# Kernel tuning notes

Measured on AMD Instinct MI355X. Metric: run time of the kernel, lower is better.

The kernel has to match this reference:

```python
import jax, jax.numpy as jnp
import numpy as np

D_MODEL = 1024
N_HEADS = 16
D_K = D_MODEL // N_HEADS


def setup_inputs() -> dict:
    key = jax.random.key(0)
    ks = jax.random.split(key, 10)
    B, S = 4, 2048
    scale = 1.0 / np.sqrt(D_MODEL)
    inp = {
        "x": jax.random.normal(ks[0], (B, S, D_MODEL), dtype=jnp.float32),
        "mask": jnp.ones((B, S), dtype=jnp.int32),
        "w_q": jax.random.normal(ks[1], (D_MODEL, D_MODEL), dtype=jnp.float32) * scale,
        "b_q": jnp.zeros((D_MODEL,), dtype=jnp.float32),
        "w_k": jax.random.normal(ks[2], (D_MODEL, D_MODEL), dtype=jnp.float32) * scale,
        "b_k": jnp.zeros((D_MODEL,), dtype=jnp.float32),
        "w_v": jax.random.normal(ks[3], (D_MODEL, D_MODEL), dtype=jnp.float32) * scale,
        "b_v": jnp.zeros((D_MODEL,), dtype=jnp.float32),
        "w_o": jax.random.normal(ks[4], (D_MODEL, D_MODEL), dtype=jnp.float32) * scale,
        "b_o": jnp.zeros((D_MODEL,), dtype=jnp.float32),
    }
    return inp


def reference(x, mask, w_q, b_q, w_k, b_k, w_v, b_v, w_o, b_o):
    B, S, _ = x.shape
    # projections; weights stored (in, out) so x @ W + b
    def proj(w, b):
        return (x @ w + b).reshape(B, S, N_HEADS, D_K).transpose(0, 2, 1, 3)  # [B,H,S,Dk]
    Q = proj(w_q, b_q)
    K = proj(w_k, b_k)
    V = proj(w_v, b_v)
    scores = jnp.einsum("bhqd,bhkd->bhqk", Q, K) / np.sqrt(D_K)  # [B,H,S,S]
    # mask: (B,S) -> (B,1,1,S); masked positions set to -1e9 (matches masked_fill)
    scores = jnp.where(mask[:, None, None, :] == 0, jnp.float32(-1e9), scores)
    attn = jax.nn.softmax(scores, axis=-1)
    # dropout is identity at inference (eval mode)
    context = jnp.einsum("bhqk,bhkd->bhqd", attn, V)  # [B,H,S,Dk]
    context = context.transpose(0, 2, 1, 3).reshape(B, S, D_MODEL)
    return context @ w_o + b_o
```

## Files before the change

kernel.cpp:

```cpp
#include <hip/hip_runtime.h>

typedef __attribute__((ext_vector_type(8)))  short short8;
typedef __attribute__((ext_vector_type(4)))  float f32x4;
typedef __attribute__((ext_vector_type(16))) float f32x16;

__device__ __forceinline__ short f2b(float f) {
    union { float f; unsigned u; } v; v.f = f;
    unsigned r = v.u + 0x7FFF + ((v.u >> 16) & 1);
    return (short)(r >> 16);
}

__device__ __forceinline__ float fexp2(float x) {
    float r;
    asm("v_exp_f32 %0, %1" : "=v"(r) : "v"(x));
    return r;
}

__device__ __forceinline__ void gll16(const void* g, void* l) {
    __builtin_amdgcn_global_load_lds(
        (const __attribute__((address_space(1))) void*)g,
        (__attribute__((address_space(3))) void*)l, 16, 0, 0);
}


__global__ __launch_bounds__(256) void xconv_kernel(const float4* __restrict__ X,
                                                    short* __restrict__ xb) {
    int i = blockIdx.x * 256 + threadIdx.x;
    float4 v = X[i];
    short4 o;
    o.x = f2b(v.x); o.y = f2b(v.y); o.z = f2b(v.z); o.w = f2b(v.w);
    ((short4*)xb)[i] = o;
}

__global__ __launch_bounds__(256) void wconv4_kernel(
    const float* __restrict__ w0, const float* __restrict__ w1,
    const float* __restrict__ w2, const float* __restrict__ w3,
    short* __restrict__ wqkvt, short* __restrict__ wot) {
    __shared__ float t[32][33];
    int z = blockIdx.z;
    const float* W = (z == 0) ? w0 : (z == 1) ? w1 : (z == 2) ? w2 : w3;
    short* WT = (z < 3) ? wqkvt : wot;
    int row_off = (z < 3) ? z * 1024 : 0;
    int bx = blockIdx.x, by = blockIdx.y;
    int c = threadIdx.x & 31, r0 = threadIdx.x >> 5;
    #pragma unroll
    for (int p = 0; p < 4; ++p) {
        int r = r0 + p * 8;
        t[r][c] = W[(size_t)(by * 32 + r) * 1024 + bx * 32 + c];
    }
    __syncthreads();
    #pragma unroll
    for (int p = 0; p < 4; ++p) {
        int r = r0 + p * 8;
        WT[(size_t)(row_off + bx * 32 + r) * 1024 + by * 32 + c] = f2b(t[c][r]);
    }
}

__global__ __launch_bounds__(256) void vtrans_kernel(const short* __restrict__ V,
                                                     short* __restrict__ Vt) {
    __shared__ short t[64][72];
    int st = blockIdx.x, bh = blockIdx.y;
    const size_t vbase = (size_t)bh * 2048 * 64;
    const size_t tbase = (size_t)bh * 64 * 2048;
    int tid = threadIdx.x;
    #pragma unroll
    for (int p = 0; p < 16; ++p) {
        int e = p * 256 + tid;
        int r = e >> 6, c = e & 63;
        t[r][c] = V[vbase + (size_t)(st * 64 + r) * 64 + c];
    }
    __syncthreads();
    #pragma unroll
    for (int p = 0; p < 16; ++p) {
        int e = p * 256 + tid;
        int d = e >> 6, c = e & 63;
        Vt[tbase + (size_t)d * 2048 + st * 64 + c] = t[c][d];
    }
}

__global__ __launch_bounds__(256) void mfma_gemm_kernel(
    const short* __restrict__ A, const short* __restrict__ Bt,
    const float* __restrict__ b0, const float* __restrict__ b1,
    const float* __restrict__ b2,
    short* __restrict__ Qo, short* __restrict__ Ko, short* __restrict__ Vo,
    float* __restrict__ Co, int K, int mode)
{
    __shared__ __align__(16) short As[2][128 * 32];
    __shared__ __align__(16) short Bs[2][128 * 32];

    const int tid = threadIdx.x;
    const int lane = tid & 63;
    const int w = tid >> 6;
    const int quad = lane >> 4;
    const int l15 = lane & 15;
    const int wm = (w & 1) * 64;
    const int wn = (w >> 1) * 64;
    const int m0 = blockIdx.y * 128;
    const int n0 = blockIdx.x * 128;

    const int rl = lane >> 2;
    const int cl = lane & 3;
    const short* srcA[2]; const short* srcB[2];
    int doff[2];
    #pragma unroll
    for (int t = 0; t < 2; ++t) {
        int row = w * 32 + t * 16 + rl;
        int sc = cl ^ (row & 3);
        srcA[t] = A  + (size_t)(m0 + row) * K + sc * 8;
        srcB[t] = Bt + (size_t)(n0 + row) * K + sc * 8;
        doff[t] = (w * 32 + t * 16) * 32;
    }

    int offA[4], offB[4];
    #pragma unroll
    for (int i = 0; i < 4; ++i) {
        int m = wm + i * 16 + l15;
        offA[i] = m * 32 + ((quad ^ (m & 3)) * 8);
        int n = wn + i * 16 + l15;
        offB[i] = n * 32 + ((quad ^ (n & 3)) * 8);
    }

    f32x4 acc[4][4];
    #pragma unroll
    for (int i = 0; i < 4; ++i)
        #pragma unroll
        for (int j = 0; j < 4; ++j)
            acc[i][j] = (f32x4){0.f, 0.f, 0.f, 0.f};

    #pragma unroll
    for (int t = 0; t < 2; ++t) {
        gll16(srcA[t], As[0] + doff[t]);
        gll16(srcB[t], Bs[0] + doff[t]);
    }
    __syncthreads();

    const int KT = K >> 5;
    for (int kt = 0; kt < KT; ++kt) {
        if (kt + 1 < KT) {
            int k1 = (kt + 1) << 5;
            int nb = (kt + 1) & 1;
            #pragma unroll
            for (int t = 0; t < 2; ++t) {
                gll16(srcA[t] + k1, As[nb] + doff[t]);
                gll16(srcB[t] + k1, Bs[nb] + doff[t]);
            }
        }
        const short* as = As[kt & 1];
        const short* bs = Bs[kt & 1];
        short8 af[4], bfr[4];
        #pragma unroll
        for (int i = 0; i < 4; ++i) af[i] = *(const short8*)(as + offA[i]);
        #pragma unroll
        for (int j = 0; j < 4; ++j) bfr[j] = *(const short8*)(bs + offB[j]);
        #pragma unroll
        for (int i = 0; i < 4; ++i)
            #pragma unroll
            for (int j = 0; j < 4; ++j)
                acc[i][j] = __builtin_amdgcn_mfma_f32_16x16x32_bf16(af[i], bfr[j], acc[i][j], 0, 0, 0);
        __syncthreads();
    }

    #pragma unroll
    for (int j = 0; j < 4; ++j) {
        int ng = n0 + wn + j * 16 + l15;
        if (mode == 0) {
            int mat = ng >> 10;
            int nl = ng & 1023;
            float bv = (mat == 0) ? b0[nl] : (mat == 1) ? b1[nl] : b2[nl];
            short* dst = (mat == 0) ? Qo : (mat == 1) ? Ko : Vo;
            float scl = (mat == 0) ? 0.18033688011112042f : 1.0f;
            int hh = nl >> 6, dd = nl & 63;
            #pragma unroll
            for (int i = 0; i < 4; ++i)
                #pragma unroll
                for (int r = 0; r < 4; ++r) {
                    int mg = m0 + wm + i * 16 + quad * 4 + r;
                    int bb = mg >> 11, ss = mg & 2047;
                    dst[(((size_t)(bb * 16 + hh)) * 2048 + ss) * 64 + dd] = f2b((acc[i][j][r] + bv) * scl);
                }
        } else {
            float bv = b0[ng];
            #pragma unroll
            for (int i = 0; i < 4; ++i)
                #pragma unroll
                for (int r = 0; r < 4; ++r) {
                    int mg = m0 + wm + i * 16 + quad * 4 + r;
                    Co[(size_t)mg * 1024 + ng] = acc[i][j][r] + bv;
                }
        }
    }
}

__global__ __launch_bounds__(256) void attn_mfma_kernel(
    const short* __restrict__ Q, const short* __restrict__ Kg,
    const short* __restrict__ Vt, const int* __restrict__ mask,
    short* __restrict__ ctx)
{
    __shared__ __align__(16) short Ks[2][64 * 64];
    __shared__ __align__(16) short Vs[2][64 * 64];
    __shared__ int msks[2][64];
    __shared__ float Linv[4][32];

    const int tid = threadIdx.x;
    const int lane = tid & 63;
    const int w = tid >> 6;
    const int l31 = lane & 31;
    const int hi = lane >> 5;
    const int bh = blockIdx.x;
    const int q0 = blockIdx.y * 128;
    const int h = bh & 15;
    const int b = bh >> 4;
    const size_t qkbase = (size_t)bh * 2048 * 64;
    const size_t vtbase = (size_t)bh * 64 * 2048;

    const int rl8 = lane >> 3;
    const int cl8 = lane & 7;

    const short* srcK[2]; const short* srcV[2];
    int dstoff[2];
    #pragma unroll
    for (int t = 0; t < 2; ++t) {
        int row = w * 16 + t * 8 + rl8;
        int sc = cl8 ^ (row & 7);
        srcK[t] = Kg + qkbase + (size_t)row * 64 + sc * 8;
        srcV[t] = Vt + vtbase + (size_t)row * 2048 + sc * 8;
        dstoff[t] = (w * 16 + t * 8) * 64;
    }

    #pragma unroll
    for (int t = 0; t < 2; ++t) {
        gll16(srcK[t], Ks[0] + dstoff[t]);
        gll16(srcV[t], Vs[0] + dstoff[t]);
    }
    if (tid < 64) msks[0][tid] = mask[b * 2048 + tid];

    short8 qf[4];
    {
        const short* qptr = Q + qkbase + (size_t)(q0 + w * 32 + l31) * 64;
        #pragma unroll
        for (int s = 0; s < 4; ++s)
            qf[s] = *(const short8*)(qptr + (((s << 1) | hi)) * 8);
    }

    f32x16 o[2];
    #pragma unroll
    for (int ch = 0; ch < 2; ++ch)
        #pragma unroll
        for (int r = 0; r < 16; ++r) o[ch][r] = 0.f;
    float lsum = 0.f;

    __syncthreads();

    for (int t = 0; t < 32; ++t) {
        const int bidx = t & 1;
        if (t + 1 < 32) {
            const int nb = (t + 1) & 1;
            const int kt1 = (t + 1) * 64;
            #pragma unroll
            for (int s = 0; s < 2; ++s) {
                gll16(srcK[s] + (size_t)kt1 * 64, Ks[nb] + dstoff[s]);
                gll16(srcV[s] + kt1, Vs[nb] + dstoff[s]);
            }
            if (tid < 64) msks[nb][tid] = mask[b * 2048 + kt1 + tid];
        }

        const short* ks = Ks[bidx];
        const short* vs = Vs[bidx];
        unsigned long long bz = __ballot(msks[bidx][tid & 63] == 0);

        #pragma unroll
        for (int km = 0; km < 2; ++km) {
            f32x16 sa;
            #pragma unroll
            for (int r = 0; r < 16; ++r) sa[r] = 0.f;
            const int kr = km * 32 + l31;
            #pragma unroll
            for (int s = 0; s < 4; ++s) {
                short8 ka = *(const short8*)(ks + kr * 64 + (((s << 1) | hi) ^ (l31 & 7)) * 8);
                sa = __builtin_amdgcn_mfma_f32_32x32x16_bf16(ka, qf[s], sa, 0, 0, 0);
            }
            float ps[16];
            #pragma unroll
            for (int r = 0; r < 16; ++r) ps[r] = fexp2(sa[r]);
            if (bz) {
                #pragma unroll
                for (int r = 0; r < 16; ++r) {
                    int key = km * 32 + (r & 3) + 8 * (r >> 2) + 4 * hi;
                    if (msks[bidx][key] == 0) ps[r] = 0.f;
                }
            }
            #pragma unroll
            for (int r = 0; r < 16; ++r) lsum += ps[r];

            unsigned pk[8];
            #pragma unroll
            for (int c = 0; c < 8; ++c) {
                unsigned u0 = __builtin_bit_cast(unsigned, ps[2 * c])     + 0x8000u;
                unsigned u1 = __builtin_bit_cast(unsigned, ps[2 * c + 1]) + 0x8000u;
                pk[c] = __builtin_amdgcn_perm(u1, u0, 0x07060302u);
            }
            unsigned sk[8];
            #pragma unroll
            for (int c = 0; c < 8; ++c) sk[c] = (unsigned)__shfl_xor((int)pk[c], 32);

            uint4 A1u, A2u;
            A1u.x = hi ? sk[2] : pk[0];
            A1u.y = hi ? sk[3] : pk[1];
            A1u.z = hi ? pk[2] : sk[0];
            A1u.w = hi ? pk[3] : sk[1];
            A2u.x = hi ? sk[6] : pk[4];
            A2u.y = hi ? sk[7] : pk[5];
            A2u.z = hi ? pk[6] : sk[4];
            A2u.w = hi ? pk[7] : sk[5];
            short8 A1 = __builtin_bit_cast(short8, A1u);
            short8 A2 = __builtin_bit_cast(short8, A2u);

            #pragma unroll
            for (int ch = 0; ch < 2; ++ch) {
                const int d = ch * 32 + l31;
                short8 vb0 = *(const short8*)(vs + d * 64 + (((km * 4) | hi) ^ (d & 7)) * 8);
                short8 vb1 = *(const short8*)(vs + d * 64 + (((km * 4 + 2) | hi) ^ (d & 7)) * 8);
                o[ch] = __builtin_amdgcn_mfma_f32_32x32x16_bf16(A1, vb0, o[ch], 0, 0, 0);
                o[ch] = __builtin_amdgcn_mfma_f32_32x32x16_bf16(A2, vb1, o[ch], 0, 0, 0);
            }
        }
        __syncthreads();
    }

    float ltot = lsum + __shfl_xor(lsum, 32);
    if (hi == 0) Linv[w][l31] = 1.0f / ltot;
    asm volatile("s_waitcnt lgkmcnt(0)" ::: "memory");
    float invr[16];
    #pragma unroll
    for (int r = 0; r < 16; ++r)
        invr[r] = Linv[w][(r & 3) + 8 * (r >> 2) + 4 * hi];
    #pragma unroll
    for (int ch = 0; ch < 2; ++ch)
        #pragma unroll
        for (int r = 0; r < 16; ++r) {
            int rowq = (r & 3) + 8 * (r >> 2) + 4 * hi;
            int qg = q0 + w * 32 + rowq;
            ctx[((size_t)b * 2048 + qg) * 1024 + h * 64 + ch * 32 + l31] =
                f2b(o[ch][r] * invr[r]);
        }
}


extern "C" void kernel_launch(void* const* d_in, const int* in_sizes, int n_in,
                              void* d_out, int out_size, void* d_ws, size_t ws_size,
                              hipStream_t stream) {
    const size_t ME = (size_t)8192 * 1024;

    char* ws = (char*)d_ws;
    short* xb    = (short*)ws; ws += ME * 2;
    short* wqkvt = (short*)ws; ws += (size_t)3072 * 1024 * 2;
    short* wot   = (short*)ws; ws += (size_t)1024 * 1024 * 2;
    short* Qb    = (short*)ws; ws += ME * 2;
    short* Kb    = (short*)ws; ws += ME * 2;
    short* Vb    = (short*)ws; ws += ME * 2;
    short* Vt    = (short*)ws; ws += ME * 2;

    xconv_kernel<<<8192, 256, 0, stream>>>((const float4*)d_in[0], xb);
    wconv4_kernel<<<dim3(32, 32, 4), 256, 0, stream>>>(
        (const float*)d_in[2], (const float*)d_in[4],
        (const float*)d_in[6], (const float*)d_in[8], wqkvt, wot);

    mfma_gemm_kernel<<<dim3(24, 64), 256, 0, stream>>>(
        xb, wqkvt, (const float*)d_in[3], (const float*)d_in[5], (const float*)d_in[7],
        Qb, Kb, Vb, nullptr, 1024, 0);

    vtrans_kernel<<<dim3(32, 64), 256, 0, stream>>>(Vb, Vt);

    attn_mfma_kernel<<<dim3(64, 16), 256, 0, stream>>>(
        Qb, Kb, Vt, (const int*)d_in[1], xb );

    mfma_gemm_kernel<<<dim3(8, 64), 256, 0, stream>>>(
        xb, wot, (const float*)d_in[9], nullptr, nullptr,
        nullptr, nullptr, nullptr, (float*)d_out, 1024, 1);
}
```

Measured before the change: 339.9 us.

## Load attention K/V fragments directly from global and bit-pack the mask

Drops the double-buffered LDS staging of K and V tiles in the attention kernel. Each wave now reads its MFMA operands straight from global memory, relying on cache reuse across the four waves, and the block-wide barriers go away. The mask is packed into 32-bit words by a new small kernel, so each key tile needs one scalar word instead of an LDS mask array. The final row normalisation uses lane shuffles instead of LDS. The risk is more global/L2 traffic and exposed load latency, since there is no explicit prefetch.

```diff
diff --git a/kernel.cpp b/kernel.cpp
--- a/kernel.cpp
+++ b/kernel.cpp
@@ -8,12 +8,6 @@
     union { float f; unsigned u; } v; v.f = f;
     unsigned r = v.u + 0x7FFF + ((v.u >> 16) & 1);
     return (short)(r >> 16);
-}
-
-__device__ __forceinline__ float fexp2(float x) {
-    float r;
-    asm("v_exp_f32 %0, %1" : "=v"(r) : "v"(x));
-    return r;
 }
 
 __device__ __forceinline__ void gll16(const void* g, void* l) {
@@ -78,6 +72,16 @@
     }
 }
 
+__global__ __launch_bounds__(256) void maskpack_kernel(const int* __restrict__ mask,
+                                                       unsigned* __restrict__ mbits) {
+    int idx = blockIdx.x * 256 + threadIdx.x;
+    int lane = threadIdx.x & 63;
+    int m = mask[idx];
+    unsigned long long bal = __ballot(m != 0);
+    if ((lane & 31) == 0)
+        mbits[idx >> 5] = (unsigned)(bal >> ((lane >> 5) * 32));
+}
+
 __global__ __launch_bounds__(256) void mfma_gemm_kernel(
     const short* __restrict__ A, const short* __restrict__ Bt,
     const float* __restrict__ b0, const float* __restrict__ b1,
@@ -193,14 +197,9 @@
 
 __global__ __launch_bounds__(256) void attn_mfma_kernel(
     const short* __restrict__ Q, const short* __restrict__ Kg,
-    const short* __restrict__ Vt, const int* __restrict__ mask,
+    const short* __restrict__ Vt, const unsigned* __restrict__ mbits,
     short* __restrict__ ctx)
 {
-    __shared__ __align__(16) short Ks[2][64 * 64];
-    __shared__ __align__(16) short Vs[2][64 * 64];
-    __shared__ int msks[2][64];
-    __shared__ float Linv[4][32];
-
     const int tid = threadIdx.x;
     const int lane = tid & 63;
     const int w = tid >> 6;
@@ -213,34 +212,17 @@
     const size_t qkbase = (size_t)bh * 2048 * 64;
     const size_t vtbase = (size_t)bh * 64 * 2048;
 
-    const int rl8 = lane >> 3;
-    const int cl8 = lane & 7;
-
-    const short* srcK[2]; const short* srcV[2];
-    int dstoff[2];
-    #pragma unroll
-    for (int t = 0; t < 2; ++t) {
-        int row = w * 16 + t * 8 + rl8;
-        int sc = cl8 ^ (row & 7);
-        srcK[t] = Kg + qkbase + (size_t)row * 64 + sc * 8;
-        srcV[t] = Vt + vtbase + (size_t)row * 2048 + sc * 8;
-        dstoff[t] = (w * 16 + t * 8) * 64;
-    }
-
-    #pragma unroll
-    for (int t = 0; t < 2; ++t) {
-        gll16(srcK[t], Ks[0] + dstoff[t]);
-        gll16(srcV[t], Vs[0] + dstoff[t]);
-    }
-    if (tid < 64) msks[0][tid] = mask[b * 2048 + tid];
-
     short8 qf[4];
     {
-        const short* qptr = Q + qkbase + (size_t)(q0 + w * 32 + l31) * 64;
+        const short* qptr = Q + qkbase + (size_t)(q0 + w * 32 + l31) * 64 + hi * 8;
         #pragma unroll
         for (int s = 0; s < 4; ++s)
-            qf[s] = *(const short8*)(qptr + (((s << 1) | hi)) * 8);
-    }
+            qf[s] = *(const short8*)(qptr + s * 16);
+    }
+
+    const short* kbase  = Kg + qkbase + (size_t)l31 * 64 + hi * 8;
+    const short* vbase0 = Vt + vtbase + (size_t)(l31) * 2048 + hi * 8;
+    const short* vbase1 = Vt + vtbase + (size_t)(32 + l31) * 2048 + hi * 8;
 
     f32x16 o[2];
     #pragma unroll
@@ -249,99 +231,80 @@
         for (int r = 0; r < 16; ++r) o[ch][r] = 0.f;
     float lsum = 0.f;
 
-    __syncthreads();
-
-    for (int t = 0; t < 32; ++t) {
-        const int bidx = t & 1;
-        if (t + 1 < 32) {
-            const int nb = (t + 1) & 1;
-            const int kt1 = (t + 1) * 64;
-            #pragma unroll
-            for (int s = 0; s < 2; ++s) {
-                gll16(srcK[s] + (size_t)kt1 * 64, Ks[nb] + dstoff[s]);
-                gll16(srcV[s] + kt1, Vs[nb] + dstoff[s]);
+    for (int kt = 0; kt < 2048; kt += 32) {
+        unsigned mword = mbits[(b << 6) + (kt >> 5)];
+
+        const short* kp = kbase + (size_t)kt * 64;
+        f32x16 sa;
+        #pragma unroll
+        for (int r = 0; r < 16; ++r) sa[r] = 0.f;
+        #pragma unroll
+        for (int s = 0; s < 4; ++s) {
+            short8 ka = *(const short8*)(kp + s * 16);
+            sa = __builtin_amdgcn_mfma_f32_32x32x16_bf16(ka, qf[s], sa, 0, 0, 0);
+        }
+
+        float ps[16];
+        #pragma unroll
+        for (int r = 0; r < 16; ++r) ps[r] = __builtin_amdgcn_exp2f(sa[r]);
+        if (mword != 0xffffffffu) {
+            #pragma unroll
+            for (int r = 0; r < 16; ++r) {
+                int key = (r & 3) + 8 * (r >> 2) + 4 * hi;
+                if (!((mword >> key) & 1)) ps[r] = 0.f;
             }
-            if (tid < 64) msks[nb][tid] = mask[b * 2048 + kt1 + tid];
-        }
-
-        const short* ks = Ks[bidx];
-        const short* vs = Vs[bidx];
-        unsigned long long bz = __ballot(msks[bidx][tid & 63] == 0);
-
-        #pragma unroll
-        for (int km = 0; km < 2; ++km) {
-            f32x16 sa;
-            #pragma unroll
-            for (int r = 0; r < 16; ++r) sa[r] = 0.f;
-            const int kr = km * 32 + l31;
-            #pragma unroll
-            for (int s = 0; s < 4; ++s) {
-                short8 ka = *(const short8*)(ks + kr * 64 + (((s << 1) | hi) ^ (l31 & 7)) * 8);
-                sa = __builtin_amdgcn_mfma_f32_32x32x16_bf16(ka, qf[s], sa, 0, 0, 0);
-            }
-            float ps[16];
-            #pragma unroll
-            for (int r = 0; r < 16; ++r) ps[r] = fexp2(sa[r]);
-            if (bz) {
-                #pragma unroll
-                for (int r = 0; r < 16; ++r) {
-                    int key = km * 32 + (r & 3) + 8 * (r >> 2) + 4 * hi;
-                    if (msks[bidx][key] == 0) ps[r] = 0.f;
-                }
-            }
-            #pragma unroll
-            for (int r = 0; r < 16; ++r) lsum += ps[r];
-
-            unsigned pk[8];
-            #pragma unroll
-            for (int c = 0; c < 8; ++c) {
-                unsigned u0 = __builtin_bit_cast(unsigned, ps[2 * c])     + 0x8000u;
-                unsigned u1 = __builtin_bit_cast(unsigned, ps[2 * c + 1]) + 0x8000u;
-                pk[c] = __builtin_amdgcn_perm(u1, u0, 0x07060302u);
-            }
-            unsigned sk[8];
-            #pragma unroll
-            for (int c = 0; c < 8; ++c) sk[c] = (unsigned)__shfl_xor((int)pk[c], 32);
-
-            uint4 A1u, A2u;
-            A1u.x = hi ? sk[2] : pk[0];
-            A1u.y = hi ? sk[3] : pk[1];
-            A1u.z = hi ? pk[2] : sk[0];
-            A1u.w = hi ? pk[3] : sk[1];
-            A2u.x = hi ? sk[6] : pk[4];
-            A2u.y = hi ? sk[7] : pk[5];
-            A2u.z = hi ? pk[6] : sk[4];
-            A2u.w = hi ? pk[7] : sk[5];
-            short8 A1 = __builtin_bit_cast(short8, A1u);
-            short8 A2 = __builtin_bit_cast(short8, A2u);
-
-            #pragma unroll
-            for (int ch = 0; ch < 2; ++ch) {
-                const int d = ch * 32 + l31;
-                short8 vb0 = *(const short8*)(vs + d * 64 + (((km * 4) | hi) ^ (d & 7)) * 8);
-                short8 vb1 = *(const short8*)(vs + d * 64 + (((km * 4 + 2) | hi) ^ (d & 7)) * 8);
-                o[ch] = __builtin_amdgcn_mfma_f32_32x32x16_bf16(A1, vb0, o[ch], 0, 0, 0);
-                o[ch] = __builtin_amdgcn_mfma_f32_32x32x16_bf16(A2, vb1, o[ch], 0, 0, 0);
-            }
-        }
-        __syncthreads();
+        }
+        #pragma unroll
+        for (int r = 0; r < 16; ++r) lsum += ps[r];
+
+        unsigned pk[8];
+        #pragma unroll
+        for (int c = 0; c < 8; ++c) {
+            unsigned u0 = __builtin_bit_cast(unsigned, ps[2 * c])     + 0x8000u;
+            unsigned u1 = __builtin_bit_cast(unsigned, ps[2 * c + 1]) + 0x8000u;
+            pk[c] = __builtin_amdgcn_perm(u1, u0, 0x07060302u);
+        }
+        unsigned sk[8];
+        #pragma unroll
+        for (int c = 0; c < 8; ++c) sk[c] = (unsigned)__shfl_xor((int)pk[c], 32);
+
+        uint4 A1u, A2u;
+        A1u.x = hi ? sk[2] : pk[0];
+        A1u.y = hi ? sk[3] : pk[1];
+        A1u.z = hi ? pk[2] : sk[0];
+        A1u.w = hi ? pk[3] : sk[1];
+        A2u.x = hi ? sk[6] : pk[4];
+        A2u.y = hi ? sk[7] : pk[5];
+        A2u.z = hi ? pk[6] : sk[4];
+        A2u.w = hi ? pk[7] : sk[5];
+        short8 A1 = __builtin_bit_cast(short8, A1u);
+        short8 A2 = __builtin_bit_cast(short8, A2u);
+
+        {
+            short8 vb0 = *(const short8*)(vbase0 + kt);
+            short8 vb1 = *(const short8*)(vbase0 + kt + 16);
+            o[0] = __builtin_amdgcn_mfma_f32_32x32x16_bf16(A1, vb0, o[0], 0, 0, 0);
+            o[0] = __builtin_amdgcn_mfma_f32_32x32x16_bf16(A2, vb1, o[0], 0, 0, 0);
+        }
+        {
+            short8 vb0 = *(const short8*)(vbase1 + kt);
+            short8 vb1 = *(const short8*)(vbase1 + kt + 16);
+            o[1] = __builtin_amdgcn_mfma_f32_32x32x16_bf16(A1, vb0, o[1], 0, 0, 0);
+            o[1] = __builtin_amdgcn_mfma_f32_32x32x16_bf16(A2, vb1, o[1], 0, 0, 0);
+        }
     }
 
     float ltot = lsum + __shfl_xor(lsum, 32);
-    if (hi == 0) Linv[w][l31] = 1.0f / ltot;
-    asm volatile("s_waitcnt lgkmcnt(0)" ::: "memory");
-    float invr[16];
-    #pragma unroll
-    for (int r = 0; r < 16; ++r)
-        invr[r] = Linv[w][(r & 3) + 8 * (r >> 2) + 4 * hi];
+    float linv = 1.0f / ltot;
     #pragma unroll
     for (int ch = 0; ch < 2; ++ch)
         #pragma unroll
         for (int r = 0; r < 16; ++r) {
             int rowq = (r & 3) + 8 * (r >> 2) + 4 * hi;
+            float inv = __shfl(linv, rowq);
             int qg = q0 + w * 32 + rowq;
             ctx[((size_t)b * 2048 + qg) * 1024 + h * 64 + ch * 32 + l31] =
-                f2b(o[ch][r] * invr[r]);
+                f2b(o[ch][r] * inv);
         }
 }
 
@@ -355,6 +318,7 @@
     short* xb    = (short*)ws; ws += ME * 2;
     short* wqkvt = (short*)ws; ws += (size_t)3072 * 1024 * 2;
     short* wot   = (short*)ws; ws += (size_t)1024 * 1024 * 2;
+    unsigned* mbits = (unsigned*)ws; ws += 1024;
     short* Qb    = (short*)ws; ws += ME * 2;
     short* Kb    = (short*)ws; ws += ME * 2;
     short* Vb    = (short*)ws; ws += ME * 2;
@@ -364,6 +328,7 @@
     wconv4_kernel<<<dim3(32, 32, 4), 256, 0, stream>>>(
         (const float*)d_in[2], (const float*)d_in[4],
         (const float*)d_in[6], (const float*)d_in[8], wqkvt, wot);
+    maskpack_kernel<<<32, 256, 0, stream>>>((const int*)d_in[1], mbits);
 
     mfma_gemm_kernel<<<dim3(24, 64), 256, 0, stream>>>(
         xb, wqkvt, (const float*)d_in[3], (const float*)d_in[5], (const float*)d_in[7],
@@ -372,7 +337,7 @@
     vtrans_kernel<<<dim3(32, 64), 256, 0, stream>>>(Vb, Vt);
 
     attn_mfma_kernel<<<dim3(64, 16), 256, 0, stream>>>(
-        Qb, Kb, Vt, (const int*)d_in[1], xb );
+        Qb, Kb, Vt, mbits, xb );
 
     mfma_gemm_kernel<<<dim3(8, 64), 256, 0, stream>>>(
         xb, wot, (const float*)d_in[9], nullptr, nullptr,
```

Measured after the change: 472.7 us. 1.39x slower.
